# Kernel optimization log

Hardware: AMD Instinct MI355X
Metric: run time of the kernel (lower is better)

The kernel has to match this reference:

```python
import jax, jax.numpy as jnp
import numpy as np
from jax.scipy.special import logsumexp

E = 512      # input_size (= 2*hidden_size)
T = 24       # output_size (num CRF tags)
B, S = 32, 512
HEADS = 2


def setup_inputs() -> dict:
    key = jax.random.key(0)
    ks = jax.random.split(key, 12)
    u = lambda k, shape, a: jax.random.uniform(k, shape, jnp.float32, -a, a)
    inp = {
        "encoder_outputs": jax.random.normal(ks[0], (B, S, E), jnp.float32),
        "labels": jax.random.randint(ks[1], (B, S), 0, T),
        "mask": jnp.ones((B, S), dtype=bool),
        # nn.MultiheadAttention params
        "Win": u(ks[2], (3 * E, E), E ** -0.5),
        "bin_": jnp.zeros((3 * E,), jnp.float32),
        "Wout": u(ks[3], (E, E), E ** -0.5),
        "bout": jnp.zeros((E,), jnp.float32),
        # crf_linear
        "crf_w": u(ks[4], (T, E), E ** -0.5),
        "crf_b": u(ks[5], (T,), E ** -0.5),
        # torchcrf CRF params (uniform(-0.1, 0.1))
        "start_t": u(ks[6], (T,), 0.1),
        "end_t": u(ks[7], (T,), 0.1),
        "trans": u(ks[8], (T, T), 0.1),
        # entity_linear
        "ent_w": u(ks[9], (2, E), E ** -0.5),
        "ent_b": u(ks[10], (2,), E ** -0.5),
    }
    return inp


def _mha(x, Win, bin_, Wout, bout):
    b, s, e = x.shape
    hd = e // HEADS
    qkv = x @ Win.T + bin_                       # [B,S,3E]
    q, k, v = jnp.split(qkv, 3, axis=-1)
    q = q.reshape(b, s, HEADS, hd)
    k = k.reshape(b, s, HEADS, hd)
    v = v.reshape(b, s, HEADS, hd)
    scores = jnp.einsum("bqhd,bkhd->bhqk", q, k) / jnp.sqrt(jnp.float32(hd))
    attn = jax.nn.softmax(scores, axis=-1)       # [B,H,S,S]
    out = jnp.einsum("bhqk,bkhd->bqhd", attn, v).reshape(b, s, e)
    return out @ Wout.T + bout


def _crf_numerator(em, labels, maskf, start_t, end_t, trans):
    # em: [B,S,T] emissions, labels: [B,S] int, maskf: [B,S] float (mask[:,0]==1)
    bidx = jnp.arange(em.shape[0])
    score = start_t[labels[:, 0]] + em[bidx, 0, labels[:, 0]]
    prev, cur = labels[:, :-1], labels[:, 1:]
    em_t = jnp.take_along_axis(em[:, 1:], cur[:, :, None], axis=2)[..., 0]
    score = score + ((trans[prev, cur] + em_t) * maskf[:, 1:]).sum(axis=1)
    seq_ends = maskf.sum(axis=1).astype(jnp.int32) - 1
    last_tags = labels[bidx, seq_ends]
    return score + end_t[last_tags]


def _crf_normalizer(em, maskf, start_t, end_t, trans):
    score0 = start_t + em[:, 0]                  # [B,T]

    def step(score, x):
        e_t, m_t = x                             # [B,T], [B]
        nxt = logsumexp(score[:, :, None] + trans[None] + e_t[:, None, :], axis=1)
        return jnp.where(m_t[:, None] > 0, nxt, score), None

    xs = (em[:, 1:].swapaxes(0, 1), maskf[:, 1:].T)
    score, _ = jax.lax.scan(step, score0, xs)
    return logsumexp(score + end_t, axis=1)


def _viterbi(em, start_t, end_t, trans):
    # decode is called without a mask -> mask of all ones
    score0 = start_t + em[:, 0]                  # [B,T]

    def step(score, e_t):
        nxt = score[:, :, None] + trans[None] + e_t[:, None, :]  # [B,T,T]
        return nxt.max(axis=1), nxt.argmax(axis=1)

    score, history = jax.lax.scan(step, score0, em[:, 1:].swapaxes(0, 1))
    last = jnp.argmax(score + end_t, axis=1)     # [B]

    def back(tag, hist):
        prev = jnp.take_along_axis(hist, tag[:, None], axis=1)[:, 0]
        return prev, prev

    _, prevs = jax.lax.scan(back, last, history, reverse=True)  # [S-1,B]
    return jnp.concatenate([prevs, last[None]], axis=0).T       # [B,S]


def reference(encoder_outputs, labels, mask, Win, bin_, Wout, bout,
              crf_w, crf_b, start_t, end_t, trans, ent_w, ent_b):
    attn = _mha(encoder_outputs, Win, bin_, Wout, bout)
    dec = jax.nn.relu(attn)                      # [B,S,E]
    fc_out = dec @ crf_w.T + crf_b               # [B,S,T]
    maskf = mask.astype(fc_out.dtype)
    num = _crf_numerator(fc_out, labels, maskf, start_t, end_t, trans)
    den = _crf_normalizer(fc_out, maskf, start_t, end_t, trans)
    llh = (num - den).sum() / maskf.sum()        # reduction='token_mean'
    crf_out = _viterbi(fc_out, start_t, end_t, trans)
    seg_out = jax.nn.log_softmax(dec @ ent_w.T + ent_b, axis=2)
    return crf_out, seg_out, -llh
```

## Files before the change

kernel.cpp:

```cpp
#include <hip/hip_runtime.h>

#define BB 32
#define SS 512
#define EE 512
#define NHH 2
#define HDD 256
#define E3 1536
#define NT 24
#define MR (BB*SS)

typedef _Float16 half8  __attribute__((ext_vector_type(8)));
typedef _Float16 half4v __attribute__((ext_vector_type(4)));
typedef float    f32x4  __attribute__((ext_vector_type(4)));

__device__ __forceinline__ float rl(float v, int l) {
    return __int_as_float(__builtin_amdgcn_readlane(__float_as_int(v), l));
}

template<int BN>
__global__ __launch_bounds__(256) void mfma_gemm(
    const float* __restrict__ A, int lda, long sAhi, long sAlo, int zA,
    const float* __restrict__ B, int ldb, long sBhi, long sBlo, int zB,
    const float* __restrict__ bias,
    float* __restrict__ C, int ldc, long sChi, long sClo, int zC,
    int K, int relu)
{
    __shared__ __align__(16) _Float16 sAh[8*640];
    __shared__ __align__(16) _Float16 sAl[8*640];
    __shared__ __align__(16) _Float16 sBh[8*640];
    __shared__ __align__(16) _Float16 sBl[8*640];

    const int t = threadIdx.x;
    const int z = blockIdx.z;
    const int za = zA + z, zb = zB + z, zc = zC + z;
    const float* Ab = A + (size_t)(za>>1)*sAhi + (size_t)(za&1)*sAlo
                        + (size_t)blockIdx.y*128*lda;
    const float* Bb = B + (size_t)(zb>>1)*sBhi + (size_t)(zb&1)*sBlo
                        + (BN ? (size_t)blockIdx.x*128
                              : (size_t)blockIdx.x*128*ldb);

    const int wv = t >> 6, lane = t & 63;
    const int wm = wv >> 1, wn = wv & 1;
    const int lm = lane & 15, lq = lane >> 4;

    f32x4 acc[4][4];
#pragma unroll
    for (int i = 0; i < 4; ++i)
#pragma unroll
        for (int j = 0; j < 4; ++j) acc[i][j] = (f32x4){0.f,0.f,0.f,0.f};

    const int r8  = t >> 3;
    const int kc  = (t & 7) * 4;
    const int bnk = (t >> 7) * 16;
    const int bnn = t & 127;

    for (int k0 = 0; k0 < K; k0 += 32) {
        float4 ga[4], gb[4]; float gv[16];
#pragma unroll
        for (int i = 0; i < 4; ++i)
            ga[i] = *(const float4*)(Ab + (size_t)(r8 + 32*i)*lda + k0 + kc);
        if (BN) {
#pragma unroll
            for (int i = 0; i < 16; ++i)
                gv[i] = Bb[(size_t)(k0 + bnk + i)*ldb + bnn];
        } else {
#pragma unroll
            for (int i = 0; i < 4; ++i)
                gb[i] = *(const float4*)(Bb + (size_t)(r8 + 32*i)*ldb + k0 + kc);
        }
        __syncthreads();
#pragma unroll
        for (int i = 0; i < 4; ++i) {
            const int row  = r8 + 32*i;
            const int base = (row >> 4)*640 + (row & 15)*40 + kc;
            float4 a = ga[i];
            _Float16 h0 = (_Float16)a.x, h1 = (_Float16)a.y,
                     h2 = (_Float16)a.z, h3 = (_Float16)a.w;
            _Float16 l0 = (_Float16)(a.x - (float)h0),
                     l1 = (_Float16)(a.y - (float)h1),
                     l2 = (_Float16)(a.z - (float)h2),
                     l3 = (_Float16)(a.w - (float)h3);
            *(half4v*)&sAh[base] = (half4v){h0,h1,h2,h3};
            *(half4v*)&sAl[base] = (half4v){l0,l1,l2,l3};
        }
        if (BN) {
#pragma unroll
            for (int i = 0; i < 16; ++i) {
                const int k = bnk + i;
                float v = gv[i];
                _Float16 h = (_Float16)v;
                _Float16 l = (_Float16)(v - (float)h);
                const int base = (bnn >> 4)*640 + (bnn & 15)*40 + k;
                sBh[base] = h;
                sBl[base] = l;
            }
        } else {
#pragma unroll
            for (int i = 0; i < 4; ++i) {
                const int row  = r8 + 32*i;
                const int base = (row >> 4)*640 + (row & 15)*40 + kc;
                float4 b = gb[i];
                _Float16 h0 = (_Float16)b.x, h1 = (_Float16)b.y,
                         h2 = (_Float16)b.z, h3 = (_Float16)b.w;
                _Float16 l0 = (_Float16)(b.x - (float)h0),
                         l1 = (_Float16)(b.y - (float)h1),
                         l2 = (_Float16)(b.z - (float)h2),
                         l3 = (_Float16)(b.w - (float)h3);
                *(half4v*)&sBh[base] = (half4v){h0,h1,h2,h3};
                *(half4v*)&sBl[base] = (half4v){l0,l1,l2,l3};
            }
        }
        __syncthreads();

        half8 bhf[4], blf[4];
#pragma unroll
        for (int j = 0; j < 4; ++j) {
            const int tb = (wn*4 + j)*640 + lm*40 + lq*8;
            bhf[j] = *(const half8*)&sBh[tb];
            blf[j] = *(const half8*)&sBl[tb];
        }
#pragma unroll
        for (int i = 0; i < 4; ++i) {
            const int ta = (wm*4 + i)*640 + lm*40 + lq*8;
            half8 ah = *(const half8*)&sAh[ta];
            half8 al = *(const half8*)&sAl[ta];
#pragma unroll
            for (int j = 0; j < 4; ++j) {
                acc[i][j] = __builtin_amdgcn_mfma_f32_16x16x32_f16(ah, bhf[j], acc[i][j], 0, 0, 0);
                acc[i][j] = __builtin_amdgcn_mfma_f32_16x16x32_f16(al, bhf[j], acc[i][j], 0, 0, 0);
                acc[i][j] = __builtin_amdgcn_mfma_f32_16x16x32_f16(ah, blf[j], acc[i][j], 0, 0, 0);
            }
        }
    }

    float* Cb = C + (size_t)(zc>>1)*sChi + (size_t)(zc&1)*sClo;
#pragma unroll
    for (int j = 0; j < 4; ++j) {
        const int col = blockIdx.x*128 + (wn*4 + j)*16 + lm;
        const float bj = bias ? bias[col] : 0.f;
#pragma unroll
        for (int i = 0; i < 4; ++i) {
            const int row0 = blockIdx.y*128 + (wm*4 + i)*16 + lq*4;
#pragma unroll
            for (int r = 0; r < 4; ++r) {
                float v = acc[i][j][r] + bj;
                if (relu) v = fmaxf(v, 0.f);
                Cb[(size_t)(row0 + r)*ldc + col] = v;
            }
        }
    }
}

__global__ __launch_bounds__(256) void softmax_rows(float* __restrict__ scores)
{
    const int w    = threadIdx.x >> 6;
    const int lane = threadIdx.x & 63;
    const size_t row = (size_t)blockIdx.x * 4 + w;
    float* p = scores + row * SS + lane * 8;
    float4 v0 = *(float4*)(p);
    float4 v1 = *(float4*)(p + 4);
    const float scale = 0.0625f;
    float m = fmaxf(fmaxf(fmaxf(v0.x, v0.y), fmaxf(v0.z, v0.w)),
                    fmaxf(fmaxf(v1.x, v1.y), fmaxf(v1.z, v1.w)));
#pragma unroll
    for (int off = 32; off >= 1; off >>= 1) m = fmaxf(m, __shfl_xor(m, off));
    v0.x = __expf((v0.x - m) * scale); v0.y = __expf((v0.y - m) * scale);
    v0.z = __expf((v0.z - m) * scale); v0.w = __expf((v0.w - m) * scale);
    v1.x = __expf((v1.x - m) * scale); v1.y = __expf((v1.y - m) * scale);
    v1.z = __expf((v1.z - m) * scale); v1.w = __expf((v1.w - m) * scale);
    float sum = v0.x + v0.y + v0.z + v0.w + v1.x + v1.y + v1.z + v1.w;
#pragma unroll
    for (int off = 32; off >= 1; off >>= 1) sum += __shfl_xor(sum, off);
    float inv = 1.f / sum;
    v0.x *= inv; v0.y *= inv; v0.z *= inv; v0.w *= inv;
    v1.x *= inv; v1.y *= inv; v1.z *= inv; v1.w *= inv;
    *(float4*)(p)     = v0;
    *(float4*)(p + 4) = v1;
}

__global__ __launch_bounds__(192) void fc_crf_kernel(
    const float* __restrict__ dec, const float* __restrict__ W,
    const float* __restrict__ bias, float* __restrict__ out)
{
    __shared__ __align__(16) float Ws[NT][516];
    for (int i = threadIdx.x; i < NT*128; i += 192) {
        int j = i >> 7, c = (i & 127) * 4;
        *(float4*)&Ws[j][c] = *(const float4*)(W + (size_t)j*EE + c);
    }
    __syncthreads();
    const int t = threadIdx.x;
    const int rloc = t / NT;
    const int j = t - rloc * NT;
    const int row = blockIdx.x * 8 + rloc;
    const float4* a = (const float4*)(dec + (size_t)row * EE);
    float acc = 0.f;
#pragma unroll 4
    for (int i = 0; i < 128; ++i) {
        float4 x = a[i];
        float4 y = *(const float4*)&Ws[j][i*4];
        acc += x.x*y.x + x.y*y.y + x.z*y.z + x.w*y.w;
    }
    out[(size_t)row * NT + j] = acc + bias[j];
}

__global__ __launch_bounds__(64, 1) void crf_seg_kernel(
    const float* __restrict__ fc, const int* __restrict__ labels,
    const float* __restrict__ start_t, const float* __restrict__ end_t,
    const float* __restrict__ trans, const float* __restrict__ dec,
    const float* __restrict__ ent_w, const float* __restrict__ ent_b,
    float* __restrict__ num, float* __restrict__ den,
    float* __restrict__ crf_out, float* __restrict__ segout)
{
    __shared__ __align__(16) float fc_lds[SS*NT];
    __shared__ unsigned char hist[(SS-1)*NT];

    const int blk  = blockIdx.x;
    const int lane = threadIdx.x;

    if (blk >= 96) {
        const int row = blk - 96;
        const float4* a  = (const float4*)(dec + (size_t)row * EE);
        const float4* w0 = (const float4*)(ent_w);
        const float4* w1 = (const float4*)(ent_w + EE);
        float acc0 = 0.f, acc1 = 0.f;
#pragma unroll
        for (int i = 0; i < 2; ++i) {
            int idx = lane * 2 + i;
            float4 x = a[idx];
            float4 u = w0[idx];
            float4 v = w1[idx];
            acc0 += x.x*u.x + x.y*u.y + x.z*u.z + x.w*u.w;
            acc1 += x.x*v.x + x.y*v.y + x.z*v.z + x.w*v.w;
        }
#pragma unroll
        for (int off = 32; off >= 1; off >>= 1) {
            acc0 += __shfl_xor(acc0, off);
            acc1 += __shfl_xor(acc1, off);
        }
        if (lane == 0) {
            float l0 = acc0 + ent_b[0];
            float l1 = acc1 + ent_b[1];
            float m  = fmaxf(l0, l1);
            float lse = m + __logf(__expf(l0 - m) + __expf(l1 - m));
            segout[(size_t)row*2 + 0] = l0 - lse;
            segout[(size_t)row*2 + 1] = l1 - lse;
        }
        return;
    }

    const int role = blk >> 5;
    const int b    = blk & 31;
    const float* fcb = fc + (size_t)b * SS * NT;

    if (role == 2) {
        float acc = 0.f;
        for (int s = 1 + lane; s < SS; s += 64) {
            int prev = labels[b*SS + s - 1];
            int cur  = labels[b*SS + s];
            acc += trans[prev*NT + cur] + fcb[(size_t)s*NT + cur];
        }
        if (lane == 0) {
            int l0 = labels[b*SS];
            acc += start_t[l0] + fcb[l0] + end_t[labels[b*SS + SS - 1]];
        }
#pragma unroll
        for (int off = 32; off >= 1; off >>= 1) acc += __shfl_xor(acc, off);
        if (lane == 0) num[b] = acc;
        return;
    }

#pragma unroll
    for (int i = 0; i < SS*NT/256; ++i) {
        const int idx = i*256 + lane*4;
        *(float4*)&fc_lds[idx] = *(const float4*)(fcb + idx);
    }
    __syncthreads();

    const int j = (lane < NT) ? lane : 0;
    float sc = start_t[j] + fc_lds[j];

    if (role == 0) {
        float etr[NT];
#pragma unroll
        for (int i = 0; i < NT; ++i) etr[i] = __expf(trans[i*NT + j]);
        float em_next = fc_lds[NT + j];
        for (int s = 1; s < SS; ++s) {
            float em = em_next;
            int snx = (s + 1 < SS) ? s + 1 : s;
            em_next = fc_lds[snx * NT + j];
            const float m  = __builtin_amdgcn_readfirstlane(sc);
            const float eo = __expf(sc - m);
            float a0 = 0.f, a1 = 0.f, a2 = 0.f, a3 = 0.f;
#pragma unroll
            for (int i = 0; i < NT; i += 4) {
                a0 = fmaf(rl(eo, i+0), etr[i+0], a0);
                a1 = fmaf(rl(eo, i+1), etr[i+1], a1);
                a2 = fmaf(rl(eo, i+2), etr[i+2], a2);
                a3 = fmaf(rl(eo, i+3), etr[i+3], a3);
            }
            sc = m + __logf((a0 + a1) + (a2 + a3)) + em;
        }
        float v = (lane < NT) ? sc + end_t[j] : -1e30f;
        float m2 = v;
#pragma unroll
        for (int off = 32; off >= 1; off >>= 1) m2 = fmaxf(m2, __shfl_xor(m2, off));
        float e = (lane < NT) ? __expf(v - m2) : 0.f;
#pragma unroll
        for (int off = 32; off >= 1; off >>= 1) e += __shfl_xor(e, off);
        if (lane == 0) den[b] = m2 + __logf(e);
    } else {
        float trC[NT];
#pragma unroll
        for (int i = 0; i < NT; ++i) trC[i] = trans[i*NT + j];
        float em_next = fc_lds[NT + j];
        for (int s = 1; s < SS; ++s) {
            float em = em_next;
            int snx = (s + 1 < SS) ? s + 1 : s;
            em_next = fc_lds[snx * NT + j];
            float tv[NT]; int ti[NT];
#pragma unroll
            for (int i = 0; i < NT; ++i) { tv[i] = rl(sc, i) + trC[i]; ti[i] = i; }
#pragma unroll
            for (int st = 1; st < NT; st <<= 1)
#pragma unroll
                for (int i = 0; i + st < NT; i += 2*st)
                    if (tv[i+st] > tv[i]) { tv[i] = tv[i+st]; ti[i] = ti[i+st]; }
            sc = tv[0] + em;
            if (lane < NT) hist[(s-1)*NT + lane] = (unsigned char)ti[0];
        }
        float bv = (lane < NT) ? sc + end_t[j] : -1e30f;
        int bi = (lane < NT) ? lane : NT;
#pragma unroll
        for (int off = 32; off >= 1; off >>= 1) {
            float ov = __shfl_xor(bv, off);
            int   oi = __shfl_xor(bi, off);
            if (ov > bv || (ov == bv && oi < bi)) { bv = ov; bi = oi; }
        }
        __syncthreads();
        if (lane == 0) {
            int tag = bi;
            crf_out[(size_t)b*SS + SS - 1] = (float)tag;
            for (int s = SS - 2; s >= 0; --s) {
                tag = hist[s*NT + tag];
                crf_out[(size_t)b*SS + s] = (float)tag;
            }
        }
    }
}

__global__ __launch_bounds__(64) void llh_kernel(
    const float* __restrict__ num, const float* __restrict__ den,
    float* __restrict__ out)
{
    int t = threadIdx.x;
    float v = (t < BB) ? (num[t] - den[t]) : 0.f;
#pragma unroll
    for (int off = 32; off >= 1; off >>= 1) v += __shfl_xor(v, off);
    if (t == 0) out[(size_t)MR * 3] = -(v / (float)MR);
}

extern "C" void kernel_launch(void* const* d_in, const int* in_sizes, int n_in,
                              void* d_out, int out_size, void* d_ws, size_t ws_size,
                              hipStream_t stream) {
    const float* enc     = (const float*)d_in[0];
    const int*   labels  = (const int*)  d_in[1];
    const float* Win     = (const float*)d_in[3];
    const float* bin     = (const float*)d_in[4];
    const float* Wout    = (const float*)d_in[5];
    const float* bout    = (const float*)d_in[6];
    const float* crf_w   = (const float*)d_in[7];
    const float* crf_b   = (const float*)d_in[8];
    const float* start_t = (const float*)d_in[9];
    const float* end_t   = (const float*)d_in[10];
    const float* trans   = (const float*)d_in[11];
    const float* ent_w   = (const float*)d_in[12];
    const float* ent_b   = (const float*)d_in[13];
    float* out = (float*)d_out;

    float* ws   = (float*)d_ws;
    float* qkv  = ws;
    float* attn = qkv  + (size_t)MR * E3;
    float* big  = attn + (size_t)MR * EE;
    float* sch  = big;
    float* dec  = big;
    float* fc   = big  + (size_t)MR * EE;
    float* num  = fc   + (size_t)MR * NT;
    float* den  = num  + BB;

    dim3 blk(256);
    mfma_gemm<0><<<dim3(E3/128, MR/128, 1), blk, 0, stream>>>(
        enc, EE, 0, 0, 0,  Win, EE, 0, 0, 0,  bin,
        qkv, E3, 0, 0, 0,  EE, 0);
    for (int p = 0; p < 2; ++p) {
        int zoff = p * 32;
        mfma_gemm<0><<<dim3(SS/128, SS/128, 32), blk, 0, stream>>>(
            qkv,      E3, (long)SS*E3, HDD, zoff,
            qkv + EE, E3, (long)SS*E3, HDD, zoff,
            nullptr,
            sch, SS, 2L*SS*SS, (long)SS*SS, 0,
            HDD, 0);
        softmax_rows<<<(32*SS)/4, blk, 0, stream>>>(sch);
        mfma_gemm<1><<<dim3(HDD/128, SS/128, 32), blk, 0, stream>>>(
            sch, SS, 2L*SS*SS, (long)SS*SS, 0,
            qkv + 2*EE, E3, (long)SS*E3, HDD, zoff,
            nullptr,
            attn, EE, (long)SS*EE, HDD, zoff,
            SS, 0);
    }
    mfma_gemm<0><<<dim3(EE/128, MR/128, 1), blk, 0, stream>>>(
        attn, EE, 0, 0, 0,  Wout, EE, 0, 0, 0,  bout,
        dec, EE, 0, 0, 0,  EE, 1);
    fc_crf_kernel<<<MR/8, dim3(192), 0, stream>>>(dec, crf_w, crf_b, fc);
    crf_seg_kernel<<<96 + MR, dim3(64), 0, stream>>>(
        fc, labels, start_t, end_t, trans, dec, ent_w, ent_b,
        num, den, out, out + MR);
    llh_kernel<<<1, 64, 0, stream>>>(num, den, out);
}
```

Measured before the change: 563.3 us.

## Split Viterbi max across wave halves, pointer-jump backtrace, batch seg rows per block

```diff
diff --git a/kernel.cpp b/kernel.cpp
--- a/kernel.cpp
+++ b/kernel.cpp
@@ -213,37 +213,47 @@
 {
     __shared__ __align__(16) float fc_lds[SS*NT];
     __shared__ unsigned char hist[(SS-1)*NT];
+    __shared__ unsigned char anchor[SS];
 
     const int blk  = blockIdx.x;
     const int lane = threadIdx.x;
 
     if (blk >= 96) {
-        const int row = blk - 96;
-        const float4* a  = (const float4*)(dec + (size_t)row * EE);
+        const int row0 = (blk - 96) * 8;
         const float4* w0 = (const float4*)(ent_w);
         const float4* w1 = (const float4*)(ent_w + EE);
-        float acc0 = 0.f, acc1 = 0.f;
-#pragma unroll
-        for (int i = 0; i < 2; ++i) {
-            int idx = lane * 2 + i;
-            float4 x = a[idx];
-            float4 u = w0[idx];
-            float4 v = w1[idx];
-            acc0 += x.x*u.x + x.y*u.y + x.z*u.z + x.w*u.w;
-            acc1 += x.x*v.x + x.y*v.y + x.z*v.z + x.w*v.w;
-        }
-#pragma unroll
-        for (int off = 32; off >= 1; off >>= 1) {
-            acc0 += __shfl_xor(acc0, off);
-            acc1 += __shfl_xor(acc1, off);
-        }
-        if (lane == 0) {
-            float l0 = acc0 + ent_b[0];
-            float l1 = acc1 + ent_b[1];
-            float m  = fmaxf(l0, l1);
-            float lse = m + __logf(__expf(l0 - m) + __expf(l1 - m));
-            segout[(size_t)row*2 + 0] = l0 - lse;
-            segout[(size_t)row*2 + 1] = l1 - lse;
+        const int i0 = lane * 2, i1 = lane * 2 + 1;
+        const float4 u0 = w0[i0], u1 = w0[i1];
+        const float4 q0 = w1[i0], q1 = w1[i1];
+        const float eb0 = ent_b[0], eb1 = ent_b[1];
+#pragma unroll 2
+        for (int r = 0; r < 8; ++r) {
+            const int row = row0 + r;
+            const float4* a = (const float4*)(dec + (size_t)row * EE);
+            float acc0 = 0.f, acc1 = 0.f;
+            {
+                float4 x = a[i0];
+                acc0 += x.x*u0.x + x.y*u0.y + x.z*u0.z + x.w*u0.w;
+                acc1 += x.x*q0.x + x.y*q0.y + x.z*q0.z + x.w*q0.w;
+            }
+            {
+                float4 x = a[i1];
+                acc0 += x.x*u1.x + x.y*u1.y + x.z*u1.z + x.w*u1.w;
+                acc1 += x.x*q1.x + x.y*q1.y + x.z*q1.z + x.w*q1.w;
+            }
+#pragma unroll
+            for (int off = 32; off >= 1; off >>= 1) {
+                acc0 += __shfl_xor(acc0, off);
+                acc1 += __shfl_xor(acc1, off);
+            }
+            if (lane == 0) {
+                float l0 = acc0 + eb0;
+                float l1 = acc1 + eb1;
+                float m  = fmaxf(l0, l1);
+                float lse = m + __logf(__expf(l0 - m) + __expf(l1 - m));
+                segout[(size_t)row*2 + 0] = l0 - lse;
+                segout[(size_t)row*2 + 1] = l1 - lse;
+            }
         }
         return;
     }
@@ -277,9 +287,9 @@
     __syncthreads();
 
     const int j = (lane < NT) ? lane : 0;
-    float sc = start_t[j] + fc_lds[j];
 
     if (role == 0) {
+        float sc = start_t[j] + fc_lds[j];
         float etr[NT];
 #pragma unroll
         for (int i = 0; i < NT; ++i) etr[i] = __expf(trans[i*NT + j]);
@@ -309,26 +319,40 @@
         for (int off = 32; off >= 1; off >>= 1) e += __shfl_xor(e, off);
         if (lane == 0) den[b] = m2 + __logf(e);
     } else {
-        float trC[NT];
-#pragma unroll
-        for (int i = 0; i < NT; ++i) trC[i] = trans[i*NT + j];
-        float em_next = fc_lds[NT + j];
+        const int jj   = lane & 31;
+        const int jc   = (jj < NT) ? jj : 0;
+        const int half = lane >> 5;
+        const int cb   = half * 12;
+
+        float trC[12];
+#pragma unroll
+        for (int ii = 0; ii < 12; ++ii) trC[ii] = trans[(cb + ii)*NT + jc];
+
+        float sc = start_t[jc] + fc_lds[jc];
+        float em_next = fc_lds[NT + jc];
         for (int s = 1; s < SS; ++s) {
             float em = em_next;
             int snx = (s + 1 < SS) ? s + 1 : s;
-            em_next = fc_lds[snx * NT + j];
-            float tv[NT]; int ti[NT];
-#pragma unroll
-            for (int i = 0; i < NT; ++i) { tv[i] = rl(sc, i) + trC[i]; ti[i] = i; }
-#pragma unroll
-            for (int st = 1; st < NT; st <<= 1)
-#pragma unroll
-                for (int i = 0; i + st < NT; i += 2*st)
+            em_next = fc_lds[snx * NT + jc];
+            float tv[12]; int ti[12];
+#pragma unroll
+            for (int ii = 0; ii < 12; ++ii) {
+                tv[ii] = __shfl(sc, cb + ii) + trC[ii];
+                ti[ii] = cb + ii;
+            }
+#pragma unroll
+            for (int st = 1; st < 12; st <<= 1)
+#pragma unroll
+                for (int i = 0; i + st < 12; i += 2*st)
                     if (tv[i+st] > tv[i]) { tv[i] = tv[i+st]; ti[i] = ti[i+st]; }
-            sc = tv[0] + em;
-            if (lane < NT) hist[(s-1)*NT + lane] = (unsigned char)ti[0];
-        }
-        float bv = (lane < NT) ? sc + end_t[j] : -1e30f;
+            float ov = __shfl_xor(tv[0], 32);
+            int   oi = __shfl_xor(ti[0], 32);
+            float bv = tv[0]; int bi2 = ti[0];
+            if (ov > bv || (ov == bv && oi < bi2)) { bv = ov; bi2 = oi; }
+            sc = bv + em;
+            if (lane < NT) hist[(s-1)*NT + lane] = (unsigned char)bi2;
+        }
+        float bv = (lane < NT) ? sc + end_t[jc] : -1e30f;
         int bi = (lane < NT) ? lane : NT;
 #pragma unroll
         for (int off = 32; off >= 1; off >>= 1) {
@@ -337,13 +361,37 @@
             if (ov > bv || (ov == bv && oi < bi)) { bv = ov; bi = oi; }
         }
         __syncthreads();
+
+        unsigned char* C0 = hist;
+        unsigned char* C1 = (unsigned char*)fc_lds;
+        if (lane < 48) {
+            const int t24 = (lane < 24) ? lane : lane - 24;
+            const int h0c = (lane < 24) ? 1 : 3;
+#pragma unroll 4
+            for (int k = 0; k < 128; ++k) {
+                int h = h0c + 4*k;
+                if (h <= 509) {
+                    int u = C0[(h+1)*NT + t24];
+                    C1[h*NT + t24] = C0[h*NT + u];
+                }
+            }
+        }
+        __syncthreads();
         if (lane == 0) {
-            int tag = bi;
-            crf_out[(size_t)b*SS + SS - 1] = (float)tag;
-            for (int s = SS - 2; s >= 0; --s) {
-                tag = hist[s*NT + tag];
-                crf_out[(size_t)b*SS + s] = (float)tag;
-            }
+            int tg = bi;
+            anchor[SS-1] = (unsigned char)tg;
+            for (int h = SS-3; h >= 1; h -= 2) {
+                tg = C1[h*NT + tg];
+                anchor[h] = (unsigned char)tg;
+            }
+        }
+        __syncthreads();
+        for (int s = lane; s < SS; s += 64) {
+            int tag;
+            if (s == SS-1)      tag = anchor[SS-1];
+            else if (s & 1)     tag = anchor[s];
+            else                tag = C0[s*NT + anchor[s+1]];
+            crf_out[(size_t)b*SS + s] = (float)tag;
         }
     }
 }
@@ -411,7 +459,7 @@
         attn, EE, 0, 0, 0,  Wout, EE, 0, 0, 0,  bout,
         dec, EE, 0, 0, 0,  EE, 1);
     fc_crf_kernel<<<MR/8, dim3(192), 0, stream>>>(dec, crf_w, crf_b, fc);
-    crf_seg_kernel<<<96 + MR, dim3(64), 0, stream>>>(
+    crf_seg_kernel<<<96 + MR/8, dim3(64), 0, stream>>>(
         fc, labels, start_t, end_t, trans, dec, ent_w, ent_b,
         num, den, out, out + MR);
     llh_kernel<<<1, 64, 0, stream>>>(num, den, out);
```

New measurement: 567.8 us. Within noise of the previous version (+0.8%).
